# Optimization experiments

Measured on AMD Instinct MI355X. Metric: run time of the kernel, lower is better.

The kernel has to match this reference:

```python
import jax, jax.numpy as jnp
import numpy as np
import math

B, S, HID, NH = 2, 1024, 4096, 32
HD = HID // NH  # 128


def setup_inputs() -> dict:
    key = jax.random.key(0)
    ks = jax.random.split(key, 6)
    scale = 0.02
    x = jax.random.normal(ks[0], (B, S, HID), dtype=jnp.float32)
    Wq = jax.random.normal(ks[1], (HID, HID), dtype=jnp.float32) * scale
    Wk = jax.random.normal(ks[2], (HID, HID), dtype=jnp.float32) * scale
    Wv = jax.random.normal(ks[3], (HID, HID), dtype=jnp.float32) * scale
    Wo = jax.random.normal(ks[4], (HID, HID), dtype=jnp.float32) * scale
    bq = jnp.zeros((HID,), jnp.float32)
    bk = jnp.zeros((HID,), jnp.float32)
    bv = jnp.zeros((HID,), jnp.float32)
    bo = jnp.zeros((HID,), jnp.float32)
    position_ids = jnp.tile(jnp.arange(S, dtype=jnp.int32)[None, :], (B, 1))
    # additive causal mask: 0 on/below diagonal, large negative above
    causal = jnp.tril(jnp.ones((S, S), dtype=bool))
    attention_mask = jnp.where(causal, 0.0, -1e9).astype(jnp.float32)[None, None]
    return {"x": x, "Wq": Wq, "bq": bq, "Wk": Wk, "bk": bk, "Wv": Wv,
            "bv": bv, "Wo": Wo, "bo": bo, "position_ids": position_ids,
            "attention_mask": attention_mask}


def _rotate_interleaved(t):
    # stack([-t[..., 1::2], t[..., ::2]], -1).reshape_as(t)
    return jnp.stack([-t[..., 1::2], t[..., ::2]], axis=-1).reshape(t.shape)


def reference(x, Wq, bq, Wk, bk, Wv, bv, Wo, bo, position_ids, attention_mask):
    b, s, _ = x.shape
    q = x @ Wq.T + bq
    k = x @ Wk.T + bk
    v = x @ Wv.T + bv
    # [B, NH, S, HD]
    q = q.reshape(b, s, NH, HD).transpose(0, 2, 1, 3)
    k = k.reshape(b, s, NH, HD).transpose(0, 2, 1, 3)
    v = v.reshape(b, s, NH, HD).transpose(0, 2, 1, 3)
    # RoPE (interleaved pairs), cos/sin recomputed each call as in source
    inv_freq = 1.0 / (10000.0 ** (jnp.arange(0, HD, 2, dtype=jnp.float32) / HD))
    ang = position_ids.astype(jnp.float32)[..., None] * inv_freq  # [B,S,HD/2]
    cos = jnp.repeat(jnp.cos(ang), 2, axis=-1)[:, None]  # [B,1,S,HD]
    sin = jnp.repeat(jnp.sin(ang), 2, axis=-1)[:, None]
    q = q * cos + _rotate_interleaved(q) * sin
    k = k * cos + _rotate_interleaved(k) * sin
    # naive full attention
    scores = jnp.einsum('bhqd,bhkd->bhqk', q, k) / math.sqrt(HD)
    scores = scores + attention_mask
    probs = jax.nn.softmax(scores, axis=-1)
    out = jnp.einsum('bhqk,bhkd->bhqd', probs, v)
    out = out.transpose(0, 2, 1, 3).reshape(b, s, HID)
    return out @ Wo.T + bo
```

## Files before the change

### kernel.cpp

```cpp
#include <hip/hip_runtime.h>
#include <hip/hip_bf16.h>
#include <cmath>

constexpr int cB  = 2;
constexpr int cS  = 1024;
constexpr int cNH = 32;
constexpr int cHD = 128;
constexpr int cHID = 4096;
constexpr int cM  = cB * cS;

typedef unsigned short u16;
typedef __bf16 bf16x8 __attribute__((ext_vector_type(8)));
typedef float  f32x4  __attribute__((ext_vector_type(4)));

__device__ __forceinline__ u16 f2b(float f) { return __builtin_bit_cast(u16, (__bf16)f); }

__global__ void cvt_bf16(const float* __restrict__ in, u16* __restrict__ out, int n8) {
  int i = blockIdx.x * blockDim.x + threadIdx.x;
  if (i >= n8) return;
  const float4* in4 = (const float4*)in;
  float4 a = in4[2 * i], b = in4[2 * i + 1];
  union { u16 u[8]; uint4 v; } r;
  r.u[0] = f2b(a.x); r.u[1] = f2b(a.y); r.u[2] = f2b(a.z); r.u[3] = f2b(a.w);
  r.u[4] = f2b(b.x); r.u[5] = f2b(b.y); r.u[6] = f2b(b.z); r.u[7] = f2b(b.w);
  ((uint4*)out)[i] = r.v;
}

__global__ void rope_table_k(const int* __restrict__ pos,
                             float* __restrict__ cosT, float* __restrict__ sinT) {
  int idx = blockIdx.x * blockDim.x + threadIdx.x;
  int i = idx & 63, bs = idx >> 6;
  float p = (float)pos[bs];
  float freq = exp2f(-(float)i * (13.287712379549449f / 64.0f));
  float a = p * freq;
  float s, c;
  sincosf(a, &s, &c);
  cosT[idx] = c; sinT[idx] = s;
}

__global__ void rope_apply(u16* __restrict__ Q, u16* __restrict__ Kb,
                           const float* __restrict__ cosT, const float* __restrict__ sinT) {
  int idx = blockIdx.x * blockDim.x + threadIdx.x;
  const int nPer = cB * cS * cNH * (cHD / 8);
  u16* P = (idx < nPer) ? Q : Kb;
  int t = (idx < nPer) ? idx : idx - nPer;
  int d8 = t & 15;
  int h  = (t >> 4) & 31;
  int bs = t >> 9;
  size_t base = ((size_t)bs * cNH + h) * cHD + d8 * 8;
  uint4 v = *reinterpret_cast<uint4*>(P + base);
  u16* u = reinterpret_cast<u16*>(&v);
  int pb = bs * 64 + d8 * 4;
  float4 cs = *reinterpret_cast<const float4*>(cosT + pb);
  float4 sn = *reinterpret_cast<const float4*>(sinT + pb);
  float co[4] = {cs.x, cs.y, cs.z, cs.w};
  float si[4] = {sn.x, sn.y, sn.z, sn.w};
#pragma unroll
  for (int p = 0; p < 4; ++p) {
    float e = (float)__builtin_bit_cast(__bf16, u[2 * p]);
    float o = (float)__builtin_bit_cast(__bf16, u[2 * p + 1]);
    float e2 = e * co[p] - o * si[p];
    float o2 = o * co[p] + e * si[p];
    u[2 * p]     = f2b(e2);
    u[2 * p + 1] = f2b(o2);
  }
  *reinterpret_cast<uint4*>(P + base) = v;
}

__global__ void transpose_v(const u16* __restrict__ V, u16* __restrict__ Vt) {
  __shared__ u16 tile[32][33];
  int bh = blockIdx.z;
  int b = bh >> 5, h = bh & 31;
  int s0 = blockIdx.x * 32, d0 = blockIdx.y * 32;
  int tx = threadIdx.x & 31, ty0 = threadIdx.x >> 5;
#pragma unroll
  for (int i = 0; i < 4; ++i) {
    int r = ty0 + i * 8;
    tile[r][tx] = V[((size_t)(b * cS + s0 + r) * cNH + h) * cHD + d0 + tx];
  }
  __syncthreads();
#pragma unroll
  for (int i = 0; i < 4; ++i) {
    int r = ty0 + i * 8;
    Vt[((size_t)bh * cHD + d0 + r) * cS + s0 + tx] = tile[tx][r];
  }
}

template <int MODE>
__global__ __launch_bounds__(512, 2)
void gemm8(const u16* __restrict__ A,
           const u16* __restrict__ W0, const u16* __restrict__ W1,
           const u16* __restrict__ W2,
           const float* __restrict__ b0, const float* __restrict__ b1,
           const float* __restrict__ b2,
           void* o0, void* o1, void* o2) {
  __shared__ __align__(16) u16 sA[3][128 * 64];
  __shared__ __align__(16) u16 sB[3][256 * 64];
  const int tid = threadIdx.x;
  const int wid = tid >> 6, lane = tid & 63;
  const int c = lane & 15, g = lane >> 4;
  const int wm = wid >> 2, wn = wid & 3;
  const int m0 = blockIdx.x * 128;
  const int gn0 = blockIdx.y * 256;
  const int sel = gn0 >> 12;
  const int n0 = gn0 & 4095;
  const u16* Bw = (sel == 0) ? W0 : (sel == 1 ? W1 : W2);

  f32x4 acc[4][4] = {};
  const int nkt = cHID / 64;

#define STAGE_A(kt, dst)                                                       \
  {                                                                            \
    _Pragma("unroll") for (int l = 0; l < 2; ++l) {                            \
      int chunk = (l * 8 + wid) * 64 + lane;                                   \
      int row = chunk >> 3, kc = (chunk & 7) ^ (row & 7);                      \
      __builtin_amdgcn_global_load_lds(                                        \
          (const void*)(A + (size_t)(m0 + row) * cHID + (kt) * 64 + kc * 8),   \
          (void*)(&sA[dst][(l * 8 + wid) * 512]), 16, 0, 0);                   \
    }                                                                          \
  }
#define STAGE_B(kt, dst)                                                       \
  {                                                                            \
    _Pragma("unroll") for (int l = 0; l < 4; ++l) {                            \
      int chunk = (l * 8 + wid) * 64 + lane;                                   \
      int row = chunk >> 3, kc = (chunk & 7) ^ (row & 7);                      \
      __builtin_amdgcn_global_load_lds(                                        \
          (const void*)(Bw + (size_t)(n0 + row) * cHID + (kt) * 64 + kc * 8),  \
          (void*)(&sB[dst][(l * 8 + wid) * 512]), 16, 0, 0);                   \
    }                                                                          \
  }

  STAGE_A(0, 0); STAGE_B(0, 0);
  STAGE_A(1, 1); STAGE_B(1, 1);
  asm volatile("s_waitcnt vmcnt(6)" ::: "memory");
  __builtin_amdgcn_sched_barrier(0);
  __builtin_amdgcn_s_barrier();
  asm volatile("" ::: "memory");
  __builtin_amdgcn_sched_barrier(0);

  for (int kt = 0; kt < nkt; ++kt) {
    const int bufR = kt % 3;
    const int bufW = (kt + 2) % 3;
    const bool doStage = (kt + 2) < nkt;

    bf16x8 af[4], bw[4];
#pragma unroll
    for (int mf = 0; mf < 4; ++mf) {
      int ra = wm * 64 + mf * 16 + c;
      af[mf] = *reinterpret_cast<const bf16x8*>(
          &sA[bufR][ra * 64 + ((g ^ (ra & 7)) * 8)]);
    }
#pragma unroll
    for (int nf = 0; nf < 4; ++nf) {
      int rb = wn * 64 + nf * 16 + c;
      bw[nf] = *reinterpret_cast<const bf16x8*>(
          &sB[bufR][rb * 64 + ((g ^ (rb & 7)) * 8)]);
    }
    if (doStage) STAGE_A(kt + 2, bufW);
    __builtin_amdgcn_s_setprio(1);
#pragma unroll
    for (int mf = 0; mf < 4; ++mf)
#pragma unroll
      for (int nf = 0; nf < 4; ++nf)
        acc[mf][nf] = __builtin_amdgcn_mfma_f32_16x16x32_bf16(af[mf], bw[nf], acc[mf][nf], 0, 0, 0);
    __builtin_amdgcn_s_setprio(0);

#pragma unroll
    for (int mf = 0; mf < 4; ++mf) {
      int ra = wm * 64 + mf * 16 + c;
      af[mf] = *reinterpret_cast<const bf16x8*>(
          &sA[bufR][ra * 64 + (((4 + g) ^ (ra & 7)) * 8)]);
    }
#pragma unroll
    for (int nf = 0; nf < 4; ++nf) {
      int rb = wn * 64 + nf * 16 + c;
      bw[nf] = *reinterpret_cast<const bf16x8*>(
          &sB[bufR][rb * 64 + (((4 + g) ^ (rb & 7)) * 8)]);
    }
    if (doStage) STAGE_B(kt + 2, bufW);
    __builtin_amdgcn_s_setprio(1);
#pragma unroll
    for (int mf = 0; mf < 4; ++mf)
#pragma unroll
      for (int nf = 0; nf < 4; ++nf)
        acc[mf][nf] = __builtin_amdgcn_mfma_f32_16x16x32_bf16(af[mf], bw[nf], acc[mf][nf], 0, 0, 0);
    __builtin_amdgcn_s_setprio(0);

    if (doStage) {
      asm volatile("s_waitcnt vmcnt(6)" ::: "memory");
    } else {
      asm volatile("s_waitcnt vmcnt(0)" ::: "memory");
    }
    __builtin_amdgcn_sched_barrier(0);
    __builtin_amdgcn_s_barrier();
    asm volatile("" ::: "memory");
    __builtin_amdgcn_sched_barrier(0);
  }
#undef STAGE_A
#undef STAGE_B

  const float* bp = (sel == 0) ? b0 : (sel == 1 ? b1 : b2);
  void* op = (sel == 0) ? o0 : (sel == 1 ? o1 : o2);
#pragma unroll
  for (int nf = 0; nf < 4; ++nf) {
    int col = n0 + wn * 64 + nf * 16 + c;
    float bv = bp[col];
#pragma unroll
    for (int mf = 0; mf < 4; ++mf) {
      int row = m0 + wm * 64 + mf * 16 + g * 4;
#pragma unroll
      for (int r = 0; r < 4; ++r) {
        float v = acc[mf][nf][r] + bv;
        if (MODE == 0)
          ((u16*)op)[(size_t)(row + r) * cHID + col] = f2b(v);
        else
          ((float*)op)[(size_t)(row + r) * cHID + col] = v;
      }
    }
  }
}

__global__ __launch_bounds__(256, 2)
void attn_kernel(const u16* __restrict__ Q, const u16* __restrict__ Kb,
                 const u16* __restrict__ Vt, u16* __restrict__ O) {
  __shared__ __align__(16) char sK[2][16384];
  __shared__ __align__(16) char sP[8192];
  const int tid = threadIdx.x, w = tid >> 6, lane = tid & 63;
  const int c = lane & 15, g = lane >> 4;
  const int bh = blockIdx.y;
  const int b = bh >> 5, h = bh & 31;
  const int NT = cS / 64;
  const int qtA = blockIdx.x, qtB = NT - 1 - blockIdx.x;
  const float kSc = 0.12751744f;
  const u16* Vg = Vt + (size_t)bh * (cHD * cS);

  bf16x8 qf[2][4];
#pragma unroll
  for (int s = 0; s < 2; ++s) {
    int q0s = (s ? qtA : qtB) * 64;
    size_t qrow = ((size_t)(b * cS + q0s + w * 16 + c) * cNH + h) * cHD;
#pragma unroll
    for (int df = 0; df < 4; ++df)
      qf[s][df] = *reinterpret_cast<const bf16x8*>(Q + qrow + df * 32 + g * 8);
  }

  f32x4 o[2][8] = {};
  float mx[2][4], ls[2][4];
#pragma unroll
  for (int s = 0; s < 2; ++s)
#pragma unroll
    for (int r = 0; r < 4; ++r) { mx[s][r] = -1e30f; ls[s][r] = 0.f; }

  uint4 kv[4];
#define LOADT(t)                                                               \
  {                                                                            \
    _Pragma("unroll") for (int i = 0; i < 4; ++i) {                            \
      int cidx = i * 256 + tid;                                                \
      int row = cidx >> 4, ch = cidx & 15;                                     \
      kv[i] = *reinterpret_cast<const uint4*>(                                 \
          Kb + ((size_t)(b * cS + (t) * 64 + row) * cNH + h) * cHD + ch * 8);  \
    }                                                                          \
  }
#define WRITET(buf)                                                            \
  {                                                                            \
    _Pragma("unroll") for (int i = 0; i < 4; ++i) {                            \
      int cidx = i * 256 + tid;                                                \
      int row = cidx >> 4, ch = cidx & 15;                                     \
      *reinterpret_cast<uint4*>(sK[buf] + row * 256 + ((ch ^ (row & 7)) * 16)) = kv[i]; \
    }                                                                          \
  }

  LOADT(0);
  WRITET(0);
  int cur = 0;

  for (int t = 0; t <= qtB; ++t) {
    __syncthreads();
    if (t < qtB) LOADT(t + 1);

#pragma unroll
    for (int s = 0; s < 2; ++s) {
      const int qt_s = s ? qtA : qtB;
      if (t > qt_s) continue;
      const int q0_s = qt_s * 64;

      f32x4 sc[4] = {};
#pragma unroll
      for (int df = 0; df < 4; ++df) {
        bf16x8 kb[4];
#pragma unroll
        for (int cf = 0; cf < 4; ++cf) {
          int kr = cf * 16 + c;
          kb[cf] = *reinterpret_cast<const bf16x8*>(sK[cur] + kr * 256 + (((df * 4 + g) ^ (kr & 7)) * 16));
        }
#pragma unroll
        for (int cf = 0; cf < 4; ++cf)
          sc[cf] = __builtin_amdgcn_mfma_f32_16x16x32_bf16(qf[s][df], kb[cf], sc[cf], 0, 0, 0);
      }

      if (t == qt_s) {
#pragma unroll
        for (int cf = 0; cf < 4; ++cf) {
          int kg = t * 64 + cf * 16 + c;
#pragma unroll
          for (int r = 0; r < 4; ++r) {
            int qg = q0_s + w * 16 + g * 4 + r;
            if (kg > qg) sc[cf][r] = -1e30f;
          }
        }
      }

      float alpha[4];
#pragma unroll
      for (int r = 0; r < 4; ++r) {
        float v = fmaxf(fmaxf(sc[0][r], sc[1][r]), fmaxf(sc[2][r], sc[3][r]));
        v = fmaxf(v, __shfl_xor(v, 1));
        v = fmaxf(v, __shfl_xor(v, 2));
        v = fmaxf(v, __shfl_xor(v, 4));
        v = fmaxf(v, __shfl_xor(v, 8));
        float mn = fmaxf(mx[s][r], v);
        alpha[r] = exp2f((mx[s][r] - mn) * kSc);
        mx[s][r] = mn;
      }
      float rs[4] = {0.f, 0.f, 0.f, 0.f};
#pragma unroll
      for (int cf = 0; cf < 4; ++cf)
#pragma unroll
        for (int r = 0; r < 4; ++r) {
          float p = exp2f((sc[cf][r] - mx[s][r]) * kSc);
          sc[cf][r] = p;
          rs[r] += p;
        }
#pragma unroll
      for (int r = 0; r < 4; ++r) {
        float v = rs[r];
        v += __shfl_xor(v, 1); v += __shfl_xor(v, 2);
        v += __shfl_xor(v, 4); v += __shfl_xor(v, 8);
        ls[s][r] = ls[s][r] * alpha[r] + v;
      }
#pragma unroll
      for (int nf = 0; nf < 8; ++nf)
#pragma unroll
        for (int r = 0; r < 4; ++r)
          o[s][nf][r] *= alpha[r];

      char* myP = sP + w * 2048;
#pragma unroll
      for (int cf = 0; cf < 4; ++cf) {
        int kcol = cf * 16 + c;
        int chunk = kcol >> 3, within = kcol & 7;
#pragma unroll
        for (int r = 0; r < 4; ++r) {
          int qr = g * 4 + r;
          *reinterpret_cast<u16*>(myP + qr * 128 + ((chunk ^ (qr & 7)) * 16) + within * 2) =
              f2b(sc[cf][r]);
        }
      }
      bf16x8 pa[2];
#pragma unroll
      for (int kf = 0; kf < 2; ++kf)
        pa[kf] = *reinterpret_cast<const bf16x8*>(myP + c * 128 + (((kf * 4 + g) ^ (c & 7)) * 16));

#pragma unroll
      for (int kf = 0; kf < 2; ++kf) {
        bf16x8 vb[8];
#pragma unroll
        for (int nf = 0; nf < 8; ++nf)
          vb[nf] = *reinterpret_cast<const bf16x8*>(
              Vg + (size_t)(nf * 16 + c) * cS + t * 64 + (kf * 4 + g) * 8);
#pragma unroll
        for (int nf = 0; nf < 8; ++nf)
          o[s][nf] = __builtin_amdgcn_mfma_f32_16x16x32_bf16(pa[kf], vb[nf], o[s][nf], 0, 0, 0);
      }
    }

    if (t < qtB) { WRITET(cur ^ 1); cur ^= 1; }
  }

  __syncthreads();
#pragma unroll
  for (int s = 0; s < 2; ++s) {
#pragma unroll
    for (int nf = 0; nf < 8; ++nf) {
#pragma unroll
      for (int r = 0; r < 4; ++r) {
        float v = o[s][nf][r] / ls[s][r];
        int qr = w * 16 + g * 4 + r;
        *reinterpret_cast<u16*>(sK[s] + qr * 256 + (nf * 16 + c) * 2) = f2b(v);
      }
    }
  }
  __syncthreads();
#pragma unroll
  for (int s = 0; s < 2; ++s) {
    int q0_s = (s ? qtA : qtB) * 64;
#pragma unroll
    for (int i = 0; i < 4; ++i) {
      int cidx = i * 256 + tid;
      int row = cidx >> 4, ch = cidx & 15;
      uint4 v = *reinterpret_cast<const uint4*>(sK[s] + row * 256 + ch * 16);
      *reinterpret_cast<uint4*>(O + ((size_t)(b * cS + q0_s + row) * cNH + h) * cHD + ch * 8) = v;
    }
  }
#undef LOADT
#undef WRITET
}

extern "C" void kernel_launch(void* const* d_in, const int* in_sizes, int n_in,
                              void* d_out, int out_size, void* d_ws, size_t ws_size,
                              hipStream_t stream) {
  const float* x  = (const float*)d_in[0];
  const float* Wq = (const float*)d_in[1];
  const float* bq = (const float*)d_in[2];
  const float* Wk = (const float*)d_in[3];
  const float* bk = (const float*)d_in[4];
  const float* Wv = (const float*)d_in[5];
  const float* bv = (const float*)d_in[6];
  const float* Wo = (const float*)d_in[7];
  const float* bo = (const float*)d_in[8];
  const int*  pos = (const int*)d_in[9];
  float* out = (float*)d_out;

  char* ws = (char*)d_ws;
  const size_t MB = 1u << 20;
  const int W8 = (cHID * cHID) / 8;
  const int X8 = (cM * cHID) / 8;
  const int R8 = cB * cS * cNH * (cHD / 8);

  if (ws_size >= 168 * MB) {
    u16* xb  = (u16*)(ws);
    u16* Qb  = (u16*)(ws + 16 * MB);
    u16* Kb  = (u16*)(ws + 32 * MB);
    u16* Vb  = (u16*)(ws + 48 * MB);
    float* cosT = (float*)(ws + 64 * MB);
    float* sinT = cosT + cB * cS * 64;
    u16* WbQ = (u16*)(ws + 72 * MB);
    u16* WbK = (u16*)(ws + 104 * MB);
    u16* WbV = (u16*)(ws + 136 * MB);
    u16* Vt  = WbQ;
    u16* Ab  = WbK;
    u16* WbO = WbV;

    cvt_bf16<<<X8 / 256, 256, 0, stream>>>(x, xb, X8);
    cvt_bf16<<<W8 / 256, 256, 0, stream>>>(Wq, WbQ, W8);
    cvt_bf16<<<W8 / 256, 256, 0, stream>>>(Wk, WbK, W8);
    cvt_bf16<<<W8 / 256, 256, 0, stream>>>(Wv, WbV, W8);
    rope_table_k<<<(cB * cS * 64) / 256, 256, 0, stream>>>(pos, cosT, sinT);

    gemm8<0><<<dim3(16, 48), 512, 0, stream>>>(
        xb, WbQ, WbK, WbV, bq, bk, bv, Qb, Kb, Vb);

    rope_apply<<<(2 * R8) / 256, 256, 0, stream>>>(Qb, Kb, cosT, sinT);
    transpose_v<<<dim3(cS / 32, cHD / 32, cB * cNH), 256, 0, stream>>>(Vb, Vt);
    attn_kernel<<<dim3(cS / 128, cB * cNH), 256, 0, stream>>>(Qb, Kb, Vt, Ab);

    cvt_bf16<<<W8 / 256, 256, 0, stream>>>(Wo, WbO, W8);
    gemm8<1><<<dim3(16, 16), 512, 0, stream>>>(
        Ab, WbO, WbO, WbO, bo, bo, bo, out, out, out);
  } else {
    u16* xb = (u16*)(ws);
    u16* Wb = (u16*)(ws + 16 * MB);
    u16* Qb = (u16*)(ws + 48 * MB);
    u16* Kb = (u16*)(ws + 64 * MB);
    u16* Vb = (u16*)(ws + 80 * MB);
    u16* Vt = xb;
    u16* Ab = Vb;
    float* cosT = (float*)(ws + 96 * MB);
    float* sinT = cosT + cB * cS * 64;

    cvt_bf16<<<X8 / 256, 256, 0, stream>>>(x, xb, X8);
    cvt_bf16<<<W8 / 256, 256, 0, stream>>>(Wq, Wb, W8);
    gemm8<0><<<dim3(16, 16), 512, 0, stream>>>(
        xb, Wb, Wb, Wb, bq, bq, bq, Qb, Qb, Qb);
    cvt_bf16<<<W8 / 256, 256, 0, stream>>>(Wk, Wb, W8);
    gemm8<0><<<dim3(16, 16), 512, 0, stream>>>(
        xb, Wb, Wb, Wb, bk, bk, bk, Kb, Kb, Kb);
    cvt_bf16<<<W8 / 256, 256, 0, stream>>>(Wv, Wb, W8);
    gemm8<0><<<dim3(16, 16), 512, 0, stream>>>(
        xb, Wb, Wb, Wb, bv, bv, bv, Vb, Vb, Vb);

    rope_table_k<<<(cB * cS * 64) / 256, 256, 0, stream>>>(pos, cosT, sinT);
    rope_apply<<<(2 * R8) / 256, 256, 0, stream>>>(Qb, Kb, cosT, sinT);
    transpose_v<<<dim3(cS / 32, cHD / 32, cB * cNH), 256, 0, stream>>>(Vb, Vt);
    attn_kernel<<<dim3(cS / 128, cB * cNH), 256, 0, stream>>>(Qb, Kb, Vt, Ab);

    cvt_bf16<<<W8 / 256, 256, 0, stream>>>(Wo, Wb, W8);
    gemm8<1><<<dim3(16, 16), 512, 0, stream>>>(
        Ab, Wb, Wb, Wb, bo, bo, bo, out, out, out);
  }
}
```

Before: 468.1 us.

## Split attention query tiles across two warp groups and merge weight conversions

The attention kernel now runs 512 threads per block, and each 4-wave group owns one of the two paired query tiles instead of one wave handling both. This halves per-thread accumulator state and should raise occupancy and parallelism, at the cost of more shared memory for P and some idle waves on the shorter tile. The three QKV weight fp32-to-bf16 conversions are merged into one launch to cut launch overhead. The V loads are also split into two batches of four to lower register pressure.

```diff
diff --git a/kernel.cpp b/kernel.cpp
--- a/kernel.cpp
+++ b/kernel.cpp
@@ -24,6 +24,21 @@
   r.u[0] = f2b(a.x); r.u[1] = f2b(a.y); r.u[2] = f2b(a.z); r.u[3] = f2b(a.w);
   r.u[4] = f2b(b.x); r.u[5] = f2b(b.y); r.u[6] = f2b(b.z); r.u[7] = f2b(b.w);
   ((uint4*)out)[i] = r.v;
+}
+
+__global__ void cvt3(const float* __restrict__ A0, const float* __restrict__ A1,
+                     const float* __restrict__ A2,
+                     u16* __restrict__ O0, u16* __restrict__ O1, u16* __restrict__ O2) {
+  int idx = blockIdx.x * blockDim.x + threadIdx.x;
+  int sel = idx >> 21, t = idx & ((1 << 21) - 1);
+  const float* in = (sel == 0) ? A0 : (sel == 1 ? A1 : A2);
+  u16* out = (sel == 0) ? O0 : (sel == 1 ? O1 : O2);
+  const float4* in4 = (const float4*)in;
+  float4 a = in4[2 * t], b = in4[2 * t + 1];
+  union { u16 u[8]; uint4 v; } rv;
+  rv.u[0] = f2b(a.x); rv.u[1] = f2b(a.y); rv.u[2] = f2b(a.z); rv.u[3] = f2b(a.w);
+  rv.u[4] = f2b(b.x); rv.u[5] = f2b(b.y); rv.u[6] = f2b(b.z); rv.u[7] = f2b(b.w);
+  ((uint4*)out)[t] = rv.v;
 }
 
 __global__ void rope_table_k(const int* __restrict__ pos,
@@ -220,42 +235,40 @@
   }
 }
 
-__global__ __launch_bounds__(256, 2)
+__global__ __launch_bounds__(512, 4)
 void attn_kernel(const u16* __restrict__ Q, const u16* __restrict__ Kb,
                  const u16* __restrict__ Vt, u16* __restrict__ O) {
   __shared__ __align__(16) char sK[2][16384];
-  __shared__ __align__(16) char sP[8192];
-  const int tid = threadIdx.x, w = tid >> 6, lane = tid & 63;
+  __shared__ __align__(16) char sP[16384];
+  const int tid = threadIdx.x, wid = tid >> 6, lane = tid & 63;
+  const int w = wid & 3, wg = wid >> 2;
   const int c = lane & 15, g = lane >> 4;
   const int bh = blockIdx.y;
   const int b = bh >> 5, h = bh & 31;
   const int NT = cS / 64;
   const int qtA = blockIdx.x, qtB = NT - 1 - blockIdx.x;
+  const int qt_s = wg ? qtA : qtB;
+  const int q0_s = qt_s * 64;
   const float kSc = 0.12751744f;
   const u16* Vg = Vt + (size_t)bh * (cHD * cS);
 
-  bf16x8 qf[2][4];
-#pragma unroll
-  for (int s = 0; s < 2; ++s) {
-    int q0s = (s ? qtA : qtB) * 64;
-    size_t qrow = ((size_t)(b * cS + q0s + w * 16 + c) * cNH + h) * cHD;
+  bf16x8 qf[4];
+  {
+    size_t qrow = ((size_t)(b * cS + q0_s + w * 16 + c) * cNH + h) * cHD;
 #pragma unroll
     for (int df = 0; df < 4; ++df)
-      qf[s][df] = *reinterpret_cast<const bf16x8*>(Q + qrow + df * 32 + g * 8);
-  }
-
-  f32x4 o[2][8] = {};
-  float mx[2][4], ls[2][4];
-#pragma unroll
-  for (int s = 0; s < 2; ++s)
-#pragma unroll
-    for (int r = 0; r < 4; ++r) { mx[s][r] = -1e30f; ls[s][r] = 0.f; }
-
-  uint4 kv[4];
+      qf[df] = *reinterpret_cast<const bf16x8*>(Q + qrow + df * 32 + g * 8);
+  }
+
+  f32x4 o[8] = {};
+  float mx[4] = {-1e30f, -1e30f, -1e30f, -1e30f};
+  float ls[4] = {0.f, 0.f, 0.f, 0.f};
+
+  uint4 kv[2];
 #define LOADT(t)                                                               \
   {                                                                            \
-    _Pragma("unroll") for (int i = 0; i < 4; ++i) {                            \
-      int cidx = i * 256 + tid;                                                \
+    _Pragma("unroll") for (int i = 0; i < 2; ++i) {                            \
+      int cidx = i * 512 + tid;                                                \
       int row = cidx >> 4, ch = cidx & 15;                                     \
       kv[i] = *reinterpret_cast<const uint4*>(                                 \
           Kb + ((size_t)(b * cS + (t) * 64 + row) * cNH + h) * cHD + ch * 8);  \
@@ -263,8 +276,8 @@
   }
 #define WRITET(buf)                                                            \
   {                                                                            \
-    _Pragma("unroll") for (int i = 0; i < 4; ++i) {                            \
-      int cidx = i * 256 + tid;                                                \
+    _Pragma("unroll") for (int i = 0; i < 2; ++i) {                            \
+      int cidx = i * 512 + tid;                                                \
       int row = cidx >> 4, ch = cidx & 15;                                     \
       *reinterpret_cast<uint4*>(sK[buf] + row * 256 + ((ch ^ (row & 7)) * 16)) = kv[i]; \
     }                                                                          \
@@ -278,12 +291,7 @@
     __syncthreads();
     if (t < qtB) LOADT(t + 1);
 
-#pragma unroll
-    for (int s = 0; s < 2; ++s) {
-      const int qt_s = s ? qtA : qtB;
-      if (t > qt_s) continue;
-      const int q0_s = qt_s * 64;
-
+    if (t <= qt_s) {
       f32x4 sc[4] = {};
 #pragma unroll
       for (int df = 0; df < 4; ++df) {
@@ -295,7 +303,7 @@
         }
 #pragma unroll
         for (int cf = 0; cf < 4; ++cf)
-          sc[cf] = __builtin_amdgcn_mfma_f32_16x16x32_bf16(qf[s][df], kb[cf], sc[cf], 0, 0, 0);
+          sc[cf] = __builtin_amdgcn_mfma_f32_16x16x32_bf16(qf[df], kb[cf], sc[cf], 0, 0, 0);
       }
 
       if (t == qt_s) {
@@ -318,16 +326,16 @@
         v = fmaxf(v, __shfl_xor(v, 2));
         v = fmaxf(v, __shfl_xor(v, 4));
         v = fmaxf(v, __shfl_xor(v, 8));
-        float mn = fmaxf(mx[s][r], v);
-        alpha[r] = exp2f((mx[s][r] - mn) * kSc);
-        mx[s][r] = mn;
+        float mn = fmaxf(mx[r], v);
+        alpha[r] = exp2f((mx[r] - mn) * kSc);
+        mx[r] = mn;
       }
       float rs[4] = {0.f, 0.f, 0.f, 0.f};
 #pragma unroll
       for (int cf = 0; cf < 4; ++cf)
 #pragma unroll
         for (int r = 0; r < 4; ++r) {
-          float p = exp2f((sc[cf][r] - mx[s][r]) * kSc);
+          float p = exp2f((sc[cf][r] - mx[r]) * kSc);
           sc[cf][r] = p;
           rs[r] += p;
         }
@@ -336,15 +344,15 @@
         float v = rs[r];
         v += __shfl_xor(v, 1); v += __shfl_xor(v, 2);
         v += __shfl_xor(v, 4); v += __shfl_xor(v, 8);
-        ls[s][r] = ls[s][r] * alpha[r] + v;
+        ls[r] = ls[r] * alpha[r] + v;
       }
 #pragma unroll
       for (int nf = 0; nf < 8; ++nf)
 #pragma unroll
         for (int r = 0; r < 4; ++r)
-          o[s][nf][r] *= alpha[r];
-
-      char* myP = sP + w * 2048;
+          o[nf][r] *= alpha[r];
+
+      char* myP = sP + wid * 2048;
 #pragma unroll
       for (int cf = 0; cf < 4; ++cf) {
         int kcol = cf * 16 + c;
@@ -363,14 +371,17 @@
 
 #pragma unroll
       for (int kf = 0; kf < 2; ++kf) {
-        bf16x8 vb[8];
-#pragma unroll
-        for (int nf = 0; nf < 8; ++nf)
-          vb[nf] = *reinterpret_cast<const bf16x8*>(
-              Vg + (size_t)(nf * 16 + c) * cS + t * 64 + (kf * 4 + g) * 8);
-#pragma unroll
-        for (int nf = 0; nf < 8; ++nf)
-          o[s][nf] = __builtin_amdgcn_mfma_f32_16x16x32_bf16(pa[kf], vb[nf], o[s][nf], 0, 0, 0);
+#pragma unroll
+        for (int h2 = 0; h2 < 2; ++h2) {
+          bf16x8 vb[4];
+#pragma unroll
+          for (int j = 0; j < 4; ++j)
+            vb[j] = *reinterpret_cast<const bf16x8*>(
+                Vg + (size_t)((h2 * 4 + j) * 16 + c) * cS + t * 64 + (kf * 4 + g) * 8);
+#pragma unroll
+          for (int j = 0; j < 4; ++j)
+            o[h2 * 4 + j] = __builtin_amdgcn_mfma_f32_16x16x32_bf16(pa[kf], vb[j], o[h2 * 4 + j], 0, 0, 0);
+        }
       }
     }
 
@@ -379,27 +390,24 @@
 
   __syncthreads();
 #pragma unroll
+  for (int nf = 0; nf < 8; ++nf) {
+#pragma unroll
+    for (int r = 0; r < 4; ++r) {
+      float v = o[nf][r] / ls[r];
+      int qr = w * 16 + g * 4 + r;
+      *reinterpret_cast<u16*>(sK[wg] + qr * 256 + (nf * 16 + c) * 2) = f2b(v);
+    }
+  }
+  __syncthreads();
+#pragma unroll
   for (int s = 0; s < 2; ++s) {
-#pragma unroll
-    for (int nf = 0; nf < 8; ++nf) {
-#pragma unroll
-      for (int r = 0; r < 4; ++r) {
-        float v = o[s][nf][r] / ls[s][r];
-        int qr = w * 16 + g * 4 + r;
-        *reinterpret_cast<u16*>(sK[s] + qr * 256 + (nf * 16 + c) * 2) = f2b(v);
-      }
-    }
-  }
-  __syncthreads();
-#pragma unroll
-  for (int s = 0; s < 2; ++s) {
-    int q0_s = (s ? qtA : qtB) * 64;
-#pragma unroll
-    for (int i = 0; i < 4; ++i) {
-      int cidx = i * 256 + tid;
+    int q0 = (s ? qtA : qtB) * 64;
+#pragma unroll
+    for (int i = 0; i < 2; ++i) {
+      int cidx = i * 512 + tid;
       int row = cidx >> 4, ch = cidx & 15;
       uint4 v = *reinterpret_cast<const uint4*>(sK[s] + row * 256 + ch * 16);
-      *reinterpret_cast<uint4*>(O + ((size_t)(b * cS + q0_s + row) * cNH + h) * cHD + ch * 8) = v;
+      *reinterpret_cast<uint4*>(O + ((size_t)(b * cS + q0 + row) * cNH + h) * cHD + ch * 8) = v;
     }
   }
 #undef LOADT
@@ -441,18 +449,16 @@
     u16* Ab  = WbK;
     u16* WbO = WbV;
 
+    cvt3<<<(3 * W8) / 256, 256, 0, stream>>>(Wq, Wk, Wv, WbQ, WbK, WbV);
+    rope_table_k<<<(cB * cS * 64) / 256, 256, 0, stream>>>(pos, cosT, sinT);
     cvt_bf16<<<X8 / 256, 256, 0, stream>>>(x, xb, X8);
-    cvt_bf16<<<W8 / 256, 256, 0, stream>>>(Wq, WbQ, W8);
-    cvt_bf16<<<W8 / 256, 256, 0, stream>>>(Wk, WbK, W8);
-    cvt_bf16<<<W8 / 256, 256, 0, stream>>>(Wv, WbV, W8);
-    rope_table_k<<<(cB * cS * 64) / 256, 256, 0, stream>>>(pos, cosT, sinT);
 
     gemm8<0><<<dim3(16, 48), 512, 0, stream>>>(
         xb, WbQ, WbK, WbV, bq, bk, bv, Qb, Kb, Vb);
 
     rope_apply<<<(2 * R8) / 256, 256, 0, stream>>>(Qb, Kb, cosT, sinT);
     transpose_v<<<dim3(cS / 32, cHD / 32, cB * cNH), 256, 0, stream>>>(Vb, Vt);
-    attn_kernel<<<dim3(cS / 128, cB * cNH), 256, 0, stream>>>(Qb, Kb, Vt, Ab);
+    attn_kernel<<<dim3(cS / 128, cB * cNH), 512, 0, stream>>>(Qb, Kb, Vt, Ab);
 
     cvt_bf16<<<W8 / 256, 256, 0, stream>>>(Wo, WbO, W8);
     gemm8<1><<<dim3(16, 16), 512, 0, stream>>>(
@@ -482,7 +488,7 @@
     rope_table_k<<<(cB * cS * 64) / 256, 256, 0, stream>>>(pos, cosT, sinT);
     rope_apply<<<(2 * R8) / 256, 256, 0, stream>>>(Qb, Kb, cosT, sinT);
     transpose_v<<<dim3(cS / 32, cHD / 32, cB * cNH), 256, 0, stream>>>(Vb, Vt);
-    attn_kernel<<<dim3(cS / 128, cB * cNH), 256, 0, stream>>>(Qb, Kb, Vt, Ab);
+    attn_kernel<<<dim3(cS / 128, cB * cNH), 512, 0, stream>>>(Qb, Kb, Vt, Ab);
 
     cvt_bf16<<<W8 / 256, 256, 0, stream>>>(Wo, Wb, W8);
     gemm8<1><<<dim3(16, 16), 512, 0, stream>>>(
```

Result: slower. 495.3 us (+5.8%).

## Fuse RoPE and V transpose into QKV GEMM epilogue, merge weight casts

Applied to the files above, without the earlier changes.

The QKV GEMM epilogue now applies interleaved RoPE to Q and K using a lane shuffle plus cos/sin table lookups, and writes V straight into the transposed [B,NH,HD,S] layout. This removes the separate rope_apply and transpose_v kernels and their extra global memory round trips. The three weight conversions are merged into one cvt3 launch to cut launch overhead. The epilogue does more gathers per element, and the transposed V stores are strided 8-byte writes, which may coalesce poorly.

```diff
diff --git a/kernel.cpp b/kernel.cpp
--- a/kernel.cpp
+++ b/kernel.cpp
@@ -24,6 +24,21 @@
   r.u[0] = f2b(a.x); r.u[1] = f2b(a.y); r.u[2] = f2b(a.z); r.u[3] = f2b(a.w);
   r.u[4] = f2b(b.x); r.u[5] = f2b(b.y); r.u[6] = f2b(b.z); r.u[7] = f2b(b.w);
   ((uint4*)out)[i] = r.v;
+}
+
+__global__ void cvt3(const float* __restrict__ A0, const float* __restrict__ A1,
+                     const float* __restrict__ A2,
+                     u16* __restrict__ O0, u16* __restrict__ O1, u16* __restrict__ O2) {
+  int idx = blockIdx.x * blockDim.x + threadIdx.x;
+  int sel = idx >> 21, t = idx & ((1 << 21) - 1);
+  const float* in = (sel == 0) ? A0 : (sel == 1 ? A1 : A2);
+  u16* out = (sel == 0) ? O0 : (sel == 1 ? O1 : O2);
+  const float4* in4 = (const float4*)in;
+  float4 a = in4[2 * t], b = in4[2 * t + 1];
+  union { u16 u[8]; uint4 v; } rv;
+  rv.u[0] = f2b(a.x); rv.u[1] = f2b(a.y); rv.u[2] = f2b(a.z); rv.u[3] = f2b(a.w);
+  rv.u[4] = f2b(b.x); rv.u[5] = f2b(b.y); rv.u[6] = f2b(b.z); rv.u[7] = f2b(b.w);
+  ((uint4*)out)[t] = rv.v;
 }
 
 __global__ void rope_table_k(const int* __restrict__ pos,
@@ -93,7 +108,8 @@
            const u16* __restrict__ W2,
            const float* __restrict__ b0, const float* __restrict__ b1,
            const float* __restrict__ b2,
-           void* o0, void* o1, void* o2) {
+           void* o0, void* o1, void* o2,
+           const float* __restrict__ cosT, const float* __restrict__ sinT) {
   __shared__ __align__(16) u16 sA[3][128 * 64];
   __shared__ __align__(16) u16 sB[3][256 * 64];
   const int tid = threadIdx.x;
@@ -201,20 +217,65 @@
 
   const float* bp = (sel == 0) ? b0 : (sel == 1 ? b1 : b2);
   void* op = (sel == 0) ? o0 : (sel == 1 ? o1 : o2);
-#pragma unroll
-  for (int nf = 0; nf < 4; ++nf) {
-    int col = n0 + wn * 64 + nf * 16 + c;
-    float bv = bp[col];
-#pragma unroll
-    for (int mf = 0; mf < 4; ++mf) {
-      int row = m0 + wm * 64 + mf * 16 + g * 4;
-#pragma unroll
-      for (int r = 0; r < 4; ++r) {
-        float v = acc[mf][nf][r] + bv;
-        if (MODE == 0)
-          ((u16*)op)[(size_t)(row + r) * cHID + col] = f2b(v);
-        else
-          ((float*)op)[(size_t)(row + r) * cHID + col] = v;
+
+  if (MODE == 0 && sel < 2) {
+#pragma unroll
+    for (int nf = 0; nf < 4; ++nf) {
+      int col = n0 + wn * 64 + nf * 16 + c;
+      float bv = bp[col];
+      int ih = (((wn & 1) * 64) + nf * 16 + c) >> 1;
+#pragma unroll
+      for (int mf = 0; mf < 4; ++mf) {
+        int row0 = m0 + wm * 64 + mf * 16 + g * 4;
+#pragma unroll
+        for (int r = 0; r < 4; ++r) {
+          int row = row0 + r;
+          float v = acc[mf][nf][r] + bv;
+          float vp = __shfl_xor(v, 1);
+          float cs = cosT[row * 64 + ih];
+          float sn = sinT[row * 64 + ih];
+          v = (c & 1) ? fmaf(vp, sn, v * cs)
+                      : fmaf(-vp, sn, v * cs);
+          ((u16*)op)[(size_t)row * cHID + col] = f2b(v);
+        }
+      }
+    }
+  } else if (MODE == 0) {
+    u16* vt = (u16*)op;
+#pragma unroll
+    for (int nf = 0; nf < 4; ++nf) {
+      int col = n0 + wn * 64 + nf * 16 + c;
+      float bv = bp[col];
+      int hh = col >> 7, dd = col & 127;
+#pragma unroll
+      for (int mf = 0; mf < 4; ++mf) {
+        int row0 = m0 + wm * 64 + mf * 16 + g * 4;
+        int bb = row0 >> 10, sl = row0 & 1023;
+        ushort4 pk;
+        pk.x = f2b(acc[mf][nf][0] + bv);
+        pk.y = f2b(acc[mf][nf][1] + bv);
+        pk.z = f2b(acc[mf][nf][2] + bv);
+        pk.w = f2b(acc[mf][nf][3] + bv);
+        *reinterpret_cast<ushort4*>(
+            vt + ((size_t)(bb * cNH + hh) * cHD + dd) * cS + sl) = pk;
+      }
+    }
+  } else {
+#pragma unroll
+    for (int nf = 0; nf < 4; ++nf) {
+      int col = n0 + wn * 64 + nf * 16 + c;
+      float bv = bp[col];
+#pragma unroll
+      for (int mf = 0; mf < 4; ++mf) {
+        int row = m0 + wm * 64 + mf * 16 + g * 4;
+#pragma unroll
+        for (int r = 0; r < 4; ++r) {
+          float v = acc[mf][nf][r] + bv;
+          if (MODE == 1)
+            ((float*)op)[(size_t)(row + r) * cHID + col] = v;
+          else
+            ((u16*)op)[(size_t)(row + r) * cHID + col] = f2b(v);
+        }
       }
     }
   }
@@ -431,32 +492,27 @@
     u16* xb  = (u16*)(ws);
     u16* Qb  = (u16*)(ws + 16 * MB);
     u16* Kb  = (u16*)(ws + 32 * MB);
-    u16* Vb  = (u16*)(ws + 48 * MB);
+    u16* Vt  = (u16*)(ws + 48 * MB);
     float* cosT = (float*)(ws + 64 * MB);
     float* sinT = cosT + cB * cS * 64;
     u16* WbQ = (u16*)(ws + 72 * MB);
     u16* WbK = (u16*)(ws + 104 * MB);
     u16* WbV = (u16*)(ws + 136 * MB);
-    u16* Vt  = WbQ;
-    u16* Ab  = WbK;
-    u16* WbO = WbV;
-
+    u16* Ab  = WbQ;
+    u16* WbO = WbK;
+
+    cvt3<<<(3 * W8) / 256, 256, 0, stream>>>(Wq, Wk, Wv, WbQ, WbK, WbV);
+    rope_table_k<<<(cB * cS * 64) / 256, 256, 0, stream>>>(pos, cosT, sinT);
     cvt_bf16<<<X8 / 256, 256, 0, stream>>>(x, xb, X8);
-    cvt_bf16<<<W8 / 256, 256, 0, stream>>>(Wq, WbQ, W8);
-    cvt_bf16<<<W8 / 256, 256, 0, stream>>>(Wk, WbK, W8);
-    cvt_bf16<<<W8 / 256, 256, 0, stream>>>(Wv, WbV, W8);
-    rope_table_k<<<(cB * cS * 64) / 256, 256, 0, stream>>>(pos, cosT, sinT);
 
     gemm8<0><<<dim3(16, 48), 512, 0, stream>>>(
-        xb, WbQ, WbK, WbV, bq, bk, bv, Qb, Kb, Vb);
-
-    rope_apply<<<(2 * R8) / 256, 256, 0, stream>>>(Qb, Kb, cosT, sinT);
-    transpose_v<<<dim3(cS / 32, cHD / 32, cB * cNH), 256, 0, stream>>>(Vb, Vt);
+        xb, WbQ, WbK, WbV, bq, bk, bv, Qb, Kb, Vt, cosT, sinT);
+
     attn_kernel<<<dim3(cS / 128, cB * cNH), 256, 0, stream>>>(Qb, Kb, Vt, Ab);
 
     cvt_bf16<<<W8 / 256, 256, 0, stream>>>(Wo, WbO, W8);
     gemm8<1><<<dim3(16, 16), 512, 0, stream>>>(
-        Ab, WbO, WbO, WbO, bo, bo, bo, out, out, out);
+        Ab, WbO, WbO, WbO, bo, bo, bo, out, out, out, nullptr, nullptr);
   } else {
     u16* xb = (u16*)(ws);
     u16* Wb = (u16*)(ws + 16 * MB);
@@ -470,14 +526,14 @@
 
     cvt_bf16<<<X8 / 256, 256, 0, stream>>>(x, xb, X8);
     cvt_bf16<<<W8 / 256, 256, 0, stream>>>(Wq, Wb, W8);
-    gemm8<0><<<dim3(16, 16), 512, 0, stream>>>(
-        xb, Wb, Wb, Wb, bq, bq, bq, Qb, Qb, Qb);
+    gemm8<3><<<dim3(16, 16), 512, 0, stream>>>(
+        xb, Wb, Wb, Wb, bq, bq, bq, Qb, Qb, Qb, nullptr, nullptr);
     cvt_bf16<<<W8 / 256, 256, 0, stream>>>(Wk, Wb, W8);
-    gemm8<0><<<dim3(16, 16), 512, 0, stream>>>(
-        xb, Wb, Wb, Wb, bk, bk, bk, Kb, Kb, Kb);
+    gemm8<3><<<dim3(16, 16), 512, 0, stream>>>(
+        xb, Wb, Wb, Wb, bk, bk, bk, Kb, Kb, Kb, nullptr, nullptr);
     cvt_bf16<<<W8 / 256, 256, 0, stream>>>(Wv, Wb, W8);
-    gemm8<0><<<dim3(16, 16), 512, 0, stream>>>(
-        xb, Wb, Wb, Wb, bv, bv, bv, Vb, Vb, Vb);
+    gemm8<3><<<dim3(16, 16), 512, 0, stream>>>(
+        xb, Wb, Wb, Wb, bv, bv, bv, Vb, Vb, Vb, nullptr, nullptr);
 
     rope_table_k<<<(cB * cS * 64) / 256, 256, 0, stream>>>(pos, cosT, sinT);
     rope_apply<<<(2 * R8) / 256, 256, 0, stream>>>(Qb, Kb, cosT, sinT);
@@ -486,6 +542,6 @@
 
     cvt_bf16<<<W8 / 256, 256, 0, stream>>>(Wo, Wb, W8);
     gemm8<1><<<dim3(16, 16), 512, 0, stream>>>(
-        Ab, Wb, Wb, Wb, bo, bo, bo, out, out, out);
-  }
-}
+        Ab, Wb, Wb, Wb, bo, bo, bo, out, out, out, nullptr, nullptr);
+  }
+}
```

New measurement: 446.5 us (median of 2 runs). -4.6%, faster.
